# Performance work log

Hardware: AMD Instinct MI355X
Metric: run time of the kernel (lower is better)

Reference implementation:

```python
import jax, jax.numpy as jnp
import numpy as np

B, N, D, H, L, FF, CLS = 32, 196, 768, 12, 12, 3072, 1000
HD = D // H
EPS = 1e-5


def setup_inputs() -> dict:
    key = jax.random.key(0)
    ks = jax.random.split(key, 8)
    s = 0.02
    return dict(
        x=jax.random.normal(ks[0], (B, N, D), jnp.float32),
        pos_emb=jax.random.normal(ks[1], (1, N, D), jnp.float32) * 0.2,
        qkv_w=jax.random.normal(ks[2], (L, D, 3 * D), jnp.float32) * s,
        qkv_b=jnp.zeros((L, 3 * D), jnp.float32),
        proj_w=jax.random.normal(ks[3], (L, D, D), jnp.float32) * s,
        proj_b=jnp.zeros((L, D), jnp.float32),
        lin1_w=jax.random.normal(ks[4], (L, D, FF), jnp.float32) * s,
        lin1_b=jnp.zeros((L, FF), jnp.float32),
        lin2_w=jax.random.normal(ks[5], (L, FF, D), jnp.float32) * s,
        lin2_b=jnp.zeros((L, D), jnp.float32),
        pre_ln_w=jnp.ones((L, D), jnp.float32),
        pre_ln_b=jnp.zeros((L, D), jnp.float32),
        norm1_w=jnp.ones((L, D), jnp.float32),
        norm1_b=jnp.zeros((L, D), jnp.float32),
        attn_ln_w=jnp.ones((L, H, N, N), jnp.float32),
        attn_ln_b=jnp.zeros((L, H, N, N), jnp.float32),
        final_ln_w=jnp.ones((D,), jnp.float32),
        final_ln_b=jnp.zeros((D,), jnp.float32),
        pool_w=jax.random.normal(ks[6], (D, 1), jnp.float32) * s,
        pool_b=jnp.zeros((1,), jnp.float32),
        fc_w=jax.random.normal(ks[7], (D, CLS), jnp.float32) * s,
        fc_b=jnp.zeros((CLS,), jnp.float32),
    )


def _ln(x, w, b):
    mu = x.mean(-1, keepdims=True)
    var = ((x - mu) ** 2).mean(-1, keepdims=True)
    return (x - mu) * jax.lax.rsqrt(var + EPS) * w + b


def _forward(x, pos_emb, qkv_w, qkv_b, proj_w, proj_b, lin1_w, lin1_b,
             lin2_w, lin2_b, pre_ln_w, pre_ln_b, norm1_w, norm1_b,
             attn_ln_w, attn_ln_b, final_ln_w, final_ln_b,
             pool_w, pool_b, fc_w, fc_b):
    h = x + pos_emb  # (B,N,D)
    params = dict(qw=qkv_w, qb=qkv_b, pw=proj_w, pb=proj_b,
                  l1w=lin1_w, l1b=lin1_b, l2w=lin2_w, l2b=lin2_b,
                  prew=pre_ln_w, preb=pre_ln_b, n1w=norm1_w, n1b=norm1_b,
                  aw=attn_ln_w, ab=attn_ln_b)

    def step(carry, p):
        src, _ = carry
        y = _ln(src, p['prew'], p['preb'])
        qkv = (y @ p['qw'] + p['qb']).reshape(B, N, 3, H, HD)
        qkv = qkv.transpose(2, 0, 3, 1, 4)  # (3,B,H,N,HD)
        q, k, v = qkv[0], qkv[1], qkv[2]
        # grassmanian_point: project each head vector onto the unit sphere
        q = q / jnp.linalg.norm(q, axis=-1, keepdims=True)
        k = k / jnp.linalg.norm(k, axis=-1, keepdims=True)
        # ||q_i outer k_j||^2 over head_dim == sum_d q_id^2 * k_jd^2
        attn = jnp.einsum('bhid,bhjd->bhij', q * q, k * k)  # (B,H,N,N)
        # LayerNorm over (H,N,N) per batch element
        mu = attn.mean(axis=(1, 2, 3), keepdims=True)
        var = ((attn - mu) ** 2).mean(axis=(1, 2, 3), keepdims=True)
        attn = (attn - mu) * jax.lax.rsqrt(var + EPS) * p['aw'] + p['ab']
        out = jnp.einsum('bhij,bhjd->bhid', attn, v)
        out = out.transpose(0, 2, 1, 3).reshape(B, N, D)
        out = out @ p['pw'] + p['pb']
        src = _ln(src + out, p['n1w'], p['n1b'])
        ff = jax.nn.gelu(src @ p['l1w'] + p['l1b'], approximate=False)
        ff = ff @ p['l2w'] + p['l2b']
        return (src + ff, attn), None

    init = (h, jnp.zeros((B, H, N, N), x.dtype))
    (src, attn), _ = jax.lax.scan(step, init, params)
    xf = _ln(src, final_ln_w, final_ln_b)
    a = jax.nn.softmax(xf @ pool_w + pool_b, axis=1)  # (B,N,1) sequence pooling
    pooled = jnp.einsum('bnk,bnd->bd', a, xf)
    logits = pooled @ fc_w + fc_b
    return logits, attn


def reference(x, pos_emb, qkv_w, qkv_b, proj_w, proj_b, lin1_w, lin1_b,
              lin2_w, lin2_b, pre_ln_w, pre_ln_b, norm1_w, norm1_b,
              attn_ln_w, attn_ln_b, final_ln_w, final_ln_b,
              pool_w, pool_b, fc_w, fc_b):
    return _forward(x, pos_emb, qkv_w, qkv_b, proj_w, proj_b, lin1_w, lin1_b,
                    lin2_w, lin2_b, pre_ln_w, pre_ln_b, norm1_w, norm1_b,
                    attn_ln_w, attn_ln_b, final_ln_w, final_ln_b,
                    pool_w, pool_b, fc_w, fc_b)
```

## Files before the change

### kernel.cpp

```cpp
#include <hip/hip_runtime.h>
#include <hip/hip_bf16.h>

typedef unsigned short u16;
typedef __bf16 bf16x8 __attribute__((ext_vector_type(8)));
typedef _Float16 f16x8 __attribute__((ext_vector_type(8)));
typedef float f32x4 __attribute__((ext_vector_type(4)));
typedef u16 u16x8 __attribute__((ext_vector_type(8)));
typedef u16 u16x4 __attribute__((ext_vector_type(4)));

#define B_ 32
#define N_ 196
#define D_ 768
#define H_ 12
#define L_ 12
#define FF_ 3072
#define CLS_ 1000
#define HD_ 64
#define BH_ 384
#define NTOK_ 6272
#define NP_ 224
#define ATTN_PER_B_ 460992
#define NN_ 38416

__device__ inline u16 f2bf(float f){
    __bf16 h = (__bf16)f;
    return __builtin_bit_cast(u16, h);
}
__device__ inline float bf2f(u16 u){
    __bf16 h = __builtin_bit_cast(__bf16, u);
    return (float)h;
}
__device__ inline void split3(float v, u16& s0, u16& s1, u16& s2){
    s0 = f2bf(v);
    float r = v - bf2f(s0);
    s1 = f2bf(r);
    r = r - bf2f(s1);
    s2 = f2bf(r);
}
__device__ inline u16 f2h(float f){
    _Float16 h = (_Float16)f;
    return __builtin_bit_cast(u16, h);
}
__device__ inline float h2f(u16 u){
    _Float16 h = __builtin_bit_cast(_Float16, u);
    return (float)h;
}
__device__ inline void split2h(float v, u16& h0, u16& h1){
    h0 = f2h(v);
    h1 = f2h(v - h2f(h0));
}


__global__ __launch_bounds__(256)
void addpos_kernel(const float* __restrict__ x, const float* __restrict__ pos,
                   float* __restrict__ src){
    size_t gid = (size_t)blockIdx.x * 256 + threadIdx.x;
    size_t e = gid * 4;
    size_t tok = e / D_;
    size_t d = e % D_;
    size_t pe = (tok % N_) * D_ + d;
    float4 a = *(const float4*)(x + e);
    float4 p = *(const float4*)(pos + pe);
    float4 o = make_float4(a.x + p.x, a.y + p.y, a.z + p.z, a.w + p.w);
    *(float4*)(src + e) = o;
}

__global__ __launch_bounds__(256)
void wtrans_kernel(const float* __restrict__ in, u16* __restrict__ o0,
                   u16* __restrict__ o1, int K, int Nn){
    __shared__ float t[32][33];
    int n0 = blockIdx.x * 32, k0 = blockIdx.y * 32;
    int tx = threadIdx.x & 31, ty = threadIdx.x >> 5;
#pragma unroll
    for (int r = 0; r < 4; ++r)
        t[ty + 8*r][tx] = in[(size_t)(k0 + ty + 8*r) * Nn + n0 + tx];
    __syncthreads();
#pragma unroll
    for (int r = 0; r < 4; ++r){
        float v = t[tx][ty + 8*r];
        size_t oi = (size_t)(n0 + ty + 8*r) * K + k0 + tx;
        u16 a, b;
        split2h(v, a, b);
        o0[oi] = a; o1[oi] = b;
    }
}


__global__ __launch_bounds__(256)
void ln_row(const float* __restrict__ in, const float* __restrict__ w,
            const float* __restrict__ bb, float* __restrict__ outF,
            u16* __restrict__ o0, u16* __restrict__ o1){
    int row = blockIdx.x, tid = threadIdx.x;
    const float* base = in + (size_t)row * D_;
    float x0 = base[tid], x1 = base[tid + 256], x2 = base[tid + 512];
    float s = x0 + x1 + x2;
    float q = x0*x0 + x1*x1 + x2*x2;
    __shared__ float red[8];
    for (int o = 32; o > 0; o >>= 1){ s += __shfl_down(s, o); q += __shfl_down(q, o); }
    if ((tid & 63) == 0){ red[tid >> 6] = s; red[4 + (tid >> 6)] = q; }
    __syncthreads();
    s = red[0] + red[1] + red[2] + red[3];
    q = red[4] + red[5] + red[6] + red[7];
    float mu = s * (1.f / D_);
    float rv = rsqrtf(q * (1.f / D_) - mu * mu + 1e-5f);
#pragma unroll
    for (int t = 0; t < 3; ++t){
        int c = tid + t * 256;
        float x = (t == 0 ? x0 : (t == 1 ? x1 : x2));
        float val = (x - mu) * rv * w[c] + bb[c];
        size_t oi = (size_t)row * D_ + c;
        if (outF) outF[oi] = val;
        if (o0){
            u16 a, b;
            split2h(val, a, b);
            o0[oi] = a; o1[oi] = b;
        }
    }
}


template<int EPI>
__global__ __launch_bounds__(256)
void gemm_f16s2(const u16* __restrict__ A0, const u16* __restrict__ A1,
                const u16* __restrict__ B0, const u16* __restrict__ B1,
                const float* __restrict__ bias, const float* __restrict__ res,
                float* __restrict__ outF, u16* __restrict__ oH,
                u16* __restrict__ oL, int M, int Nn, int K){
    __shared__ u16 Lds[2][4][128 * 32];
    const int tid = threadIdx.x;
    const int w = tid >> 6, l = tid & 63;
    const int wr = w >> 1, wc = w & 1;
    const int nwg = gridDim.x;
    const int nbx = Nn >> 7;
    const int orig = blockIdx.x;
    const int qq = nwg >> 3, rr = nwg & 7;
    const int xcd = orig & 7, local = orig >> 3;
    const int wg = (xcd < rr ? xcd * (qq + 1) : rr * (qq + 1) + (xcd - rr) * qq) + local;
    const int m0 = (wg / nbx) * 128, n0 = (wg % nbx) * 128;
    const u16* gsrc = (w == 0 ? A0 : w == 1 ? A1 : w == 2 ? B0 : B1);
    const int rowbase = (w < 2 ? m0 : n0);
    const int lq = (l & 3) ^ ((l >> 3) & 3);
    const u16* gp = gsrc + (size_t)(rowbase + (l >> 2)) * K + lq * 8;
    const size_t gstep = (size_t)16 * K;
    f32x4 acc[4][4] = {};
    const int arow = l & 15;
    const int qsel = l >> 4;
    const int nsteps = K >> 5;

    auto stage = [&](int buf, int k0){
        u16* lbuf = &Lds[buf][w][0];
        const u16* gpk = gp + k0;
#pragma unroll
        for (int i = 0; i < 8; ++i){
            __builtin_amdgcn_global_load_lds(
                (const __attribute__((address_space(1))) unsigned int*)gpk,
                (__attribute__((address_space(3))) unsigned int*)(lbuf + i * 512),
                16, 0, 0);
            gpk += gstep;
        }
    };

    stage(0, 0);
    for (int step = 0; step < nsteps; ++step){
        const int cur = step & 1;
        __syncthreads();
        if (step + 1 < nsteps) stage(1 - cur, (step + 1) << 5);
        f16x8 a0[4], a1[4], b0[4], b1[4];
#pragma unroll
        for (int m = 0; m < 4; ++m){
            int row = wr * 64 + m * 16 + arow;
            int off = row * 32 + ((qsel ^ ((row >> 1) & 3)) * 8);
            a0[m] = __builtin_bit_cast(f16x8, *(const u16x8*)&Lds[cur][0][off]);
            a1[m] = __builtin_bit_cast(f16x8, *(const u16x8*)&Lds[cur][1][off]);
        }
#pragma unroll
        for (int n = 0; n < 4; ++n){
            int row = wc * 64 + n * 16 + arow;
            int off = row * 32 + ((qsel ^ ((row >> 1) & 3)) * 8);
            b0[n] = __builtin_bit_cast(f16x8, *(const u16x8*)&Lds[cur][2][off]);
            b1[n] = __builtin_bit_cast(f16x8, *(const u16x8*)&Lds[cur][3][off]);
        }
#pragma unroll
        for (int m = 0; m < 4; ++m)
#pragma unroll
            for (int n = 0; n < 4; ++n){
                acc[m][n] = __builtin_amdgcn_mfma_f32_16x16x32_f16(a1[m], b0[n], acc[m][n], 0, 0, 0);
                acc[m][n] = __builtin_amdgcn_mfma_f32_16x16x32_f16(a0[m], b1[n], acc[m][n], 0, 0, 0);
                acc[m][n] = __builtin_amdgcn_mfma_f32_16x16x32_f16(a0[m], b0[n], acc[m][n], 0, 0, 0);
            }
    }
    const int r4 = (l >> 4) * 4, c16 = l & 15;
#pragma unroll
    for (int m = 0; m < 4; ++m){
#pragma unroll
        for (int n = 0; n < 4; ++n){
            int colg = n0 + wc*64 + n*16 + c16;
            float bv = bias[colg];
#pragma unroll
            for (int r = 0; r < 4; ++r){
                int rowg = m0 + wr*64 + m*16 + r4 + r;
                size_t oi = (size_t)rowg * Nn + colg;
                float v = acc[m][n][r] + bv;
                if (EPI == 0){
                    outF[oi] = v;
                } else if (EPI == 1){
                    v = 0.5f * v * (1.0f + erff(v * 0.70710678118654752f));
                    u16 a, b;
                    split2h(v, a, b);
                    oH[oi] = a; oL[oi] = b;
                } else {
                    outF[oi] = v + res[oi];
                }
            }
        }
    }
}


__global__ __launch_bounds__(256)
void qkprep_kernel(const float* __restrict__ QKV,
                   u16* __restrict__ Q0, u16* __restrict__ Q1, u16* __restrict__ Q2,
                   u16* __restrict__ K0, u16* __restrict__ K1, u16* __restrict__ K2,
                   u16* __restrict__ VT0, u16* __restrict__ VT1, u16* __restrict__ VT2){
    __shared__ float vbuf[NP_][65];
    int bh = blockIdx.x;
    int b = bh / H_, h = bh % H_;
    int w = threadIdx.x >> 6, l = threadIdx.x & 63;
    size_t base = (size_t)bh * (NP_ * HD_);
    for (int n = w; n < NP_; n += 4){
        size_t oi = base + (size_t)n * HD_ + l;
        if (n < N_){
            const float* row = QKV + (size_t)(b * N_ + n) * (3 * D_) + h * HD_;
            float qv = row[l], kv = row[D_ + l], vv = row[2 * D_ + l];
            double qs = (double)qv * (double)qv, ks = (double)kv * (double)kv;
            double qr = qs, kr = ks;
            for (int o = 32; o > 0; o >>= 1){ qr += __shfl_xor(qr, o); kr += __shfl_xor(kr, o); }
            float q2 = (float)(qs / qr), k2 = (float)(ks / kr);
            u16 a, bb, c;
            split3(q2, a, bb, c);
            Q0[oi] = a; Q1[oi] = bb; Q2[oi] = c;
            split3(k2, a, bb, c);
            K0[oi] = a; K1[oi] = bb; K2[oi] = c;
            vbuf[n][l] = vv;
        } else {
            Q0[oi] = 0; Q1[oi] = 0; Q2[oi] = 0;
            K0[oi] = 0; K1[oi] = 0; K2[oi] = 0;
            vbuf[n][l] = 0.f;
        }
    }
    __syncthreads();
    size_t vtb = (size_t)bh * (HD_ * NP_);
    for (int idx = threadIdx.x; idx < HD_ * NP_; idx += 256){
        int d = idx / NP_, n = idx % NP_;
        u16 a, bb, c;
        split3(vbuf[n][d], a, bb, c);
        VT0[vtb + idx] = a; VT1[vtb + idx] = bb; VT2[vtb + idx] = c;
    }
}


#define SPAD 72

__global__ __launch_bounds__(256)
void score_mfma3(const u16* __restrict__ Q0, const u16* __restrict__ Q1,
                 const u16* __restrict__ Q2,
                 const u16* __restrict__ K0, const u16* __restrict__ K1,
                 const u16* __restrict__ K2,
                 float* __restrict__ S){
    __shared__ u16 Ql[3][32][SPAD];
    __shared__ u16 Kl[3][32][SPAD];
    int i0 = blockIdx.x * 32;
    int bh = blockIdx.y;
    int tid = threadIdx.x;
    size_t base = (size_t)bh * (NP_ * HD_);
    {
        int r = tid >> 3, q = tid & 7;
        size_t src = base + (size_t)(i0 + r) * HD_ + q * 8;
        *(u16x8*)&Ql[0][r][q * 8] = *(const u16x8*)(Q0 + src);
        *(u16x8*)&Ql[1][r][q * 8] = *(const u16x8*)(Q1 + src);
        *(u16x8*)&Ql[2][r][q * 8] = *(const u16x8*)(Q2 + src);
    }
    const int w = tid >> 6, l = tid & 63;
    const int wm = w >> 1, wn = w & 1;
    const int arow = l & 15, kg0 = (l >> 4) * 8;
    const int r4 = (l >> 4) * 4, c16 = l & 15;
    for (int jt = 0; jt < 7; ++jt){
        __syncthreads();
        {
            int r = tid >> 3, q = tid & 7;
            size_t src = base + (size_t)(jt * 32 + r) * HD_ + q * 8;
            *(u16x8*)&Kl[0][r][q * 8] = *(const u16x8*)(K0 + src);
            *(u16x8*)&Kl[1][r][q * 8] = *(const u16x8*)(K1 + src);
            *(u16x8*)&Kl[2][r][q * 8] = *(const u16x8*)(K2 + src);
        }
        __syncthreads();
        f32x4 acc = {};
#pragma unroll
        for (int kk = 0; kk < 2; ++kk){
            int kg = kk * 32 + kg0;
            bf16x8 a0 = __builtin_bit_cast(bf16x8, *(const u16x8*)&Ql[0][wm*16 + arow][kg]);
            bf16x8 a1 = __builtin_bit_cast(bf16x8, *(const u16x8*)&Ql[1][wm*16 + arow][kg]);
            bf16x8 a2 = __builtin_bit_cast(bf16x8, *(const u16x8*)&Ql[2][wm*16 + arow][kg]);
            bf16x8 b0 = __builtin_bit_cast(bf16x8, *(const u16x8*)&Kl[0][wn*16 + arow][kg]);
            bf16x8 b1 = __builtin_bit_cast(bf16x8, *(const u16x8*)&Kl[1][wn*16 + arow][kg]);
            bf16x8 b2 = __builtin_bit_cast(bf16x8, *(const u16x8*)&Kl[2][wn*16 + arow][kg]);
            acc = __builtin_amdgcn_mfma_f32_16x16x32_bf16(a2, b0, acc, 0, 0, 0);
            acc = __builtin_amdgcn_mfma_f32_16x16x32_bf16(a1, b1, acc, 0, 0, 0);
            acc = __builtin_amdgcn_mfma_f32_16x16x32_bf16(a0, b2, acc, 0, 0, 0);
            acc = __builtin_amdgcn_mfma_f32_16x16x32_bf16(a1, b0, acc, 0, 0, 0);
            acc = __builtin_amdgcn_mfma_f32_16x16x32_bf16(a0, b1, acc, 0, 0, 0);
            acc = __builtin_amdgcn_mfma_f32_16x16x32_bf16(a0, b0, acc, 0, 0, 0);
        }
#pragma unroll
        for (int r = 0; r < 4; ++r){
            int i = i0 + wm * 16 + r4 + r;
            int j = jt * 32 + wn * 16 + c16;
            if (i < N_ && j < N_)
                S[((size_t)bh * N_ + i) * N_ + j] = acc[r];
        }
    }
}


__global__ __launch_bounds__(256)
void statsA_kernel(const float* __restrict__ S, double* __restrict__ part1){
    int b = blockIdx.y, c = blockIdx.x;
    const float* base = S + (size_t)b * ATTN_PER_B_ + (size_t)c * 7203;
    double s = 0.0;
    for (int i = threadIdx.x; i < 7203; i += 256)
        s += (double)base[i];
    __shared__ double red[4];
    for (int o = 32; o > 0; o >>= 1) s += __shfl_down(s, o);
    if ((threadIdx.x & 63) == 0) red[threadIdx.x >> 6] = s;
    __syncthreads();
    if (threadIdx.x == 0) part1[b * 64 + c] = red[0] + red[1] + red[2] + red[3];
}

__global__ __launch_bounds__(64)
void reduceMu_kernel(const double* __restrict__ part1, double* __restrict__ MU){
    int b = blockIdx.x;
    double s = part1[b * 64 + threadIdx.x];
    for (int o = 32; o > 0; o >>= 1) s += __shfl_down(s, o);
    if (threadIdx.x == 0) MU[b] = s / (double)ATTN_PER_B_;
}

__global__ __launch_bounds__(256)
void statsB_kernel(const float* __restrict__ S, const double* __restrict__ MU,
                   double* __restrict__ part2){
    int b = blockIdx.y, c = blockIdx.x;
    double mu = MU[b];
    const float* base = S + (size_t)b * ATTN_PER_B_ + (size_t)c * 7203;
    double q = 0.0;
    for (int i = threadIdx.x; i < 7203; i += 256){
        double d = (double)base[i] - mu;
        q += d * d;
    }
    __shared__ double red[4];
    for (int o = 32; o > 0; o >>= 1) q += __shfl_down(q, o);
    if ((threadIdx.x & 63) == 0) red[threadIdx.x >> 6] = q;
    __syncthreads();
    if (threadIdx.x == 0) part2[b * 64 + c] = red[0] + red[1] + red[2] + red[3];
}

__global__ __launch_bounds__(64)
void reduceR_kernel(const double* __restrict__ part2, const double* __restrict__ MU,
                    float2* __restrict__ musig){
    int b = blockIdx.x;
    double q = part2[b * 64 + threadIdx.x];
    for (int o = 32; o > 0; o >>= 1) q += __shfl_down(q, o);
    if (threadIdx.x == 0){
        double var = q / (double)ATTN_PER_B_;
        musig[b] = make_float2((float)MU[b], (float)(1.0 / sqrt(var + 1e-5)));
    }
}


__global__ __launch_bounds__(256)
void attnnorm_pad(float* __restrict__ S, const float* __restrict__ wv,
                  const float* __restrict__ bv, const float2* __restrict__ musig,
                  u16* __restrict__ AS0, u16* __restrict__ AS1, u16* __restrict__ AS2){
    int gid = blockIdx.x * 256 + threadIdx.x;
    int jg = gid % 56;
    int rem = gid / 56;
    int i = rem % NP_;
    int bh = rem / NP_;
    int b = bh / H_, h = bh % H_;
    float2 ms = musig[b];
    u16x4 p0, p1, p2;
#pragma unroll
    for (int t = 0; t < 4; ++t){
        int j = jg * 4 + t;
        float val = 0.f;
        if (i < N_ && j < N_){
            size_t si = ((size_t)bh * N_ + i) * N_ + j;
            size_t wi = ((size_t)h * N_ + i) * N_ + j;
            float s = S[si];
            val = (s - ms.x) * ms.y * wv[wi] + bv[wi];
            S[si] = val;
        }
        u16 a, bb, c;
        split3(val, a, bb, c);
        p0[t] = a; p1[t] = bb; p2[t] = c;
    }
    size_t oo = (size_t)bh * (NP_ * NP_) + (size_t)i * NP_ + jg * 4;
    *(u16x4*)&AS0[oo] = p0;
    *(u16x4*)&AS1[oo] = p1;
    *(u16x4*)&AS2[oo] = p2;
}


__global__ __launch_bounds__(256)
void pv_mfma3(const u16* __restrict__ AS0, const u16* __restrict__ AS1,
              const u16* __restrict__ AS2,
              const u16* __restrict__ VT0, const u16* __restrict__ VT1,
              const u16* __restrict__ VT2,
              u16* __restrict__ PA0, u16* __restrict__ PA1){
    __shared__ u16 Al[3][32][40];
    __shared__ u16 Vl[3][64][40];
    int i0 = blockIdx.x * 32;
    int bh = blockIdx.y;
    int b = bh / H_, h = bh % H_;
    int tid = threadIdx.x;
    size_t abase = (size_t)bh * (NP_ * NP_) + (size_t)i0 * NP_;
    size_t vbase = (size_t)bh * (HD_ * NP_);
    const int w = tid >> 6, l = tid & 63;
    const int arow = l & 15, kg0 = (l >> 4) * 8;
    const int r4 = (l >> 4) * 4, c16 = l & 15;
    f32x4 acc[2] = {};
    for (int k0 = 0; k0 < NP_; k0 += 32){
        __syncthreads();
        for (int c = tid; c < 384; c += 256){
            int s = c >> 7, rem = c & 127;
            int r = rem >> 2, q = rem & 3;
            const u16* src = (s == 0 ? AS0 : (s == 1 ? AS1 : AS2));
            *(u16x8*)&Al[s][r][q * 8] = *(const u16x8*)(src + abase + (size_t)r * NP_ + k0 + q * 8);
        }
        for (int c = tid; c < 768; c += 256){
            int s = c >> 8, rem = c & 255;
            int r = rem >> 2, q = rem & 3;
            const u16* src = (s == 0 ? VT0 : (s == 1 ? VT1 : VT2));
            *(u16x8*)&Vl[s][r][q * 8] = *(const u16x8*)(src + vbase + (size_t)r * NP_ + k0 + q * 8);
        }
        __syncthreads();
        bf16x8 a0[2], a1[2], a2[2];
#pragma unroll
        for (int m = 0; m < 2; ++m){
            a0[m] = __builtin_bit_cast(bf16x8, *(const u16x8*)&Al[0][m*16 + arow][kg0]);
            a1[m] = __builtin_bit_cast(bf16x8, *(const u16x8*)&Al[1][m*16 + arow][kg0]);
            a2[m] = __builtin_bit_cast(bf16x8, *(const u16x8*)&Al[2][m*16 + arow][kg0]);
        }
        bf16x8 b0 = __builtin_bit_cast(bf16x8, *(const u16x8*)&Vl[0][w*16 + arow][kg0]);
        bf16x8 b1 = __builtin_bit_cast(bf16x8, *(const u16x8*)&Vl[1][w*16 + arow][kg0]);
        bf16x8 b2 = __builtin_bit_cast(bf16x8, *(const u16x8*)&Vl[2][w*16 + arow][kg0]);
#pragma unroll
        for (int m = 0; m < 2; ++m){
            acc[m] = __builtin_amdgcn_mfma_f32_16x16x32_bf16(a2[m], b0, acc[m], 0, 0, 0);
            acc[m] = __builtin_amdgcn_mfma_f32_16x16x32_bf16(a1[m], b1, acc[m], 0, 0, 0);
            acc[m] = __builtin_amdgcn_mfma_f32_16x16x32_bf16(a0[m], b2, acc[m], 0, 0, 0);
            acc[m] = __builtin_amdgcn_mfma_f32_16x16x32_bf16(a1[m], b0, acc[m], 0, 0, 0);
            acc[m] = __builtin_amdgcn_mfma_f32_16x16x32_bf16(a0[m], b1, acc[m], 0, 0, 0);
            acc[m] = __builtin_amdgcn_mfma_f32_16x16x32_bf16(a0[m], b0, acc[m], 0, 0, 0);
        }
    }
#pragma unroll
    for (int m = 0; m < 2; ++m)
#pragma unroll
        for (int r = 0; r < 4; ++r){
            int i = i0 + m * 16 + r4 + r;
            if (i < N_){
                size_t oi = ((size_t)b * N_ + i) * D_ + h * HD_ + w * 16 + c16;
                u16 s0, s1;
                split2h(acc[m][r], s0, s1);
                PA0[oi] = s0; PA1[oi] = s1;
            }
        }
}


__global__ __launch_bounds__(256)
void rowdot_kernel(const float* __restrict__ xf, const float* __restrict__ pw,
                   const float* __restrict__ pb, float* __restrict__ sraw){
    int row = blockIdx.x, tid = threadIdx.x;
    const float* base = xf + (size_t)row * D_;
    float s = base[tid] * pw[tid] + base[tid + 256] * pw[tid + 256] + base[tid + 512] * pw[tid + 512];
    __shared__ float red[4];
    for (int o = 32; o > 0; o >>= 1) s += __shfl_xor(s, o);
    if ((tid & 63) == 0) red[tid >> 6] = s;
    __syncthreads();
    if (tid == 0) sraw[row] = red[0] + red[1] + red[2] + red[3] + pb[0];
}

__global__ __launch_bounds__(256)
void softmax196_kernel(const float* __restrict__ sraw, float* __restrict__ aw){
    int b = blockIdx.x, tid = threadIdx.x;
    __shared__ float red[8];
    float v = (tid < N_) ? sraw[b * N_ + tid] : -3.0e38f;
    float m = v;
    for (int o = 32; o > 0; o >>= 1) m = fmaxf(m, __shfl_xor(m, o));
    if ((tid & 63) == 0) red[tid >> 6] = m;
    __syncthreads();
    float M = fmaxf(fmaxf(red[0], red[1]), fmaxf(red[2], red[3]));
    float e = (tid < N_) ? expf(v - M) : 0.f;
    float s = e;
    for (int o = 32; o > 0; o >>= 1) s += __shfl_xor(s, o);
    if ((tid & 63) == 0) red[4 + (tid >> 6)] = s;
    __syncthreads();
    float S = red[4] + red[5] + red[6] + red[7];
    if (tid < N_) aw[b * N_ + tid] = e / S;
}

__global__ __launch_bounds__(256)
void poolmat_kernel(const float* __restrict__ aw, const float* __restrict__ xf,
                    float* __restrict__ pooled){
    int b = blockIdx.y;
    int d = blockIdx.x * 256 + threadIdx.x;
    float acc = 0.f;
    for (int n = 0; n < N_; ++n)
        acc += aw[b * N_ + n] * xf[((size_t)b * N_ + n) * D_ + d];
    pooled[b * D_ + d] = acc;
}

__global__ __launch_bounds__(256)
void fc_kernel(const float* __restrict__ pooled, const float* __restrict__ fw,
               const float* __restrict__ fb, float* __restrict__ out){
    int b = blockIdx.y;
    int c = blockIdx.x * 256 + threadIdx.x;
    if (c >= CLS_) return;
    float acc = fb[c];
    for (int d = 0; d < D_; ++d)
        acc += pooled[b * D_ + d] * fw[(size_t)d * CLS_ + c];
    out[b * CLS_ + c] = acc;
}

__global__ __launch_bounds__(256)
void zero_logits(float* __restrict__ out){
    out[blockIdx.x * 256 + threadIdx.x] = 0.f;
}


extern "C" void kernel_launch(void* const* d_in, const int* in_sizes, int n_in,
                              void* d_out, int out_size, void* d_ws, size_t ws_size,
                              hipStream_t stream){
    const float* x        = (const float*)d_in[0];
    const float* pos_emb  = (const float*)d_in[1];
    const float* qkv_w    = (const float*)d_in[2];
    const float* qkv_b    = (const float*)d_in[3];
    const float* proj_w   = (const float*)d_in[4];
    const float* proj_b   = (const float*)d_in[5];
    const float* lin1_w   = (const float*)d_in[6];
    const float* lin1_b   = (const float*)d_in[7];
    const float* lin2_w   = (const float*)d_in[8];
    const float* lin2_b   = (const float*)d_in[9];
    const float* pre_ln_w = (const float*)d_in[10];
    const float* pre_ln_b = (const float*)d_in[11];
    const float* norm1_w  = (const float*)d_in[12];
    const float* norm1_b  = (const float*)d_in[13];
    const float* attn_ln_w= (const float*)d_in[14];
    const float* attn_ln_b= (const float*)d_in[15];
    const float* fln_w    = (const float*)d_in[16];
    const float* fln_b    = (const float*)d_in[17];
    const float* pool_w   = (const float*)d_in[18];
    const float* pool_b   = (const float*)d_in[19];
    const float* fc_w     = (const float*)d_in[20];
    const float* fc_b     = (const float*)d_in[21];

    float* dout = (float*)d_out;
    float* S = dout + (size_t)B_ * CLS_;

    char* ws = (char*)d_ws;
    size_t off = 0;
    auto alloc = [&](size_t bytes)->char*{
        char* p = ws + off;
        off += (bytes + 255) & ~(size_t)255;
        return p;
    };
    float* SRC   = (float*)alloc((size_t)NTOK_ * D_ * 4);
    float* Yb    = (float*)alloc((size_t)NTOK_ * D_ * 4);
    float* TMP   = (float*)alloc((size_t)NTOK_ * D_ * 4);
    float* QKV   = (float*)alloc((size_t)NTOK_ * 3 * D_ * 4);
    u16*   A0    = (u16*)  alloc((size_t)NTOK_ * D_ * 2);
    u16*   A1    = (u16*)  alloc((size_t)NTOK_ * D_ * 2);
    u16*   W0    = (u16*)  alloc((size_t)FF_ * D_ * 2);
    u16*   W1    = (u16*)  alloc((size_t)FF_ * D_ * 2);
    u16*   F0    = (u16*)  alloc((size_t)NTOK_ * FF_ * 2);
    u16*   F1    = (u16*)  alloc((size_t)NTOK_ * FF_ * 2);
    u16*   F2    = (u16*)  alloc((size_t)NTOK_ * FF_ * 2);
    u16*   Q0b   = (u16*)  alloc((size_t)BH_ * NP_ * HD_ * 2);
    u16*   Q1b   = (u16*)  alloc((size_t)BH_ * NP_ * HD_ * 2);
    u16*   Q2b   = (u16*)  alloc((size_t)BH_ * NP_ * HD_ * 2);
    u16*   K0b   = (u16*)  alloc((size_t)BH_ * NP_ * HD_ * 2);
    u16*   K1b   = (u16*)  alloc((size_t)BH_ * NP_ * HD_ * 2);
    u16*   K2b   = (u16*)  alloc((size_t)BH_ * NP_ * HD_ * 2);
    u16*   VT0   = (u16*)  alloc((size_t)BH_ * HD_ * NP_ * 2);
    u16*   VT1   = (u16*)  alloc((size_t)BH_ * HD_ * NP_ * 2);
    u16*   VT2   = (u16*)  alloc((size_t)BH_ * HD_ * NP_ * 2);
    double* P1   = (double*)alloc((size_t)B_ * 64 * 8);
    double* P2   = (double*)alloc((size_t)B_ * 64 * 8);
    double* MU   = (double*)alloc((size_t)B_ * 8);
    float2* MUSIG= (float2*)alloc((size_t)B_ * 8);
    float* SRAW  = (float*)alloc((size_t)NTOK_ * 4);
    float* AW    = (float*)alloc((size_t)NTOK_ * 4);
    float* POOLED= (float*)alloc((size_t)B_ * D_ * 4);
    u16* AS0 = F0, *AS1 = F1, *AS2 = F2;

    if (ws_size < off){
        zero_logits<<<(B_ * CLS_) / 256, 256, 0, stream>>>(dout);
        return;
    }

    const int cvt_blocks = NTOK_ * D_ / (256 * 4);
    const int an_blocks = (int)((size_t)BH_ * NP_ * NP_ / (256 * 4));

    addpos_kernel<<<cvt_blocks, 256, 0, stream>>>(x, pos_emb, SRC);

    for (int l = 0; l < L_; ++l){
        const float* qw  = qkv_w  + (size_t)l * D_ * 3 * D_;
        const float* qb  = qkv_b  + (size_t)l * 3 * D_;
        const float* pw  = proj_w + (size_t)l * D_ * D_;
        const float* pb  = proj_b + (size_t)l * D_;
        const float* l1w = lin1_w + (size_t)l * D_ * FF_;
        const float* l1b = lin1_b + (size_t)l * FF_;
        const float* l2w = lin2_w + (size_t)l * FF_ * D_;
        const float* l2b = lin2_b + (size_t)l * D_;
        const float* prw = pre_ln_w + (size_t)l * D_;
        const float* prb = pre_ln_b + (size_t)l * D_;
        const float* n1w = norm1_w + (size_t)l * D_;
        const float* n1b = norm1_b + (size_t)l * D_;
        const float* awl = attn_ln_w + (size_t)l * H_ * N_ * N_;
        const float* abl = attn_ln_b + (size_t)l * H_ * N_ * N_;

        ln_row<<<NTOK_, 256, 0, stream>>>(SRC, prw, prb, nullptr, A0, A1);
        wtrans_kernel<<<dim3(3 * D_ / 32, D_ / 32), 256, 0, stream>>>(qw, W0, W1, D_, 3 * D_);
        gemm_f16s2<0><<<(3 * D_ / 128) * (NTOK_ / 128), 256, 0, stream>>>(
            A0, A1, W0, W1, qb, nullptr, QKV, nullptr, nullptr, NTOK_, 3 * D_, D_);
        qkprep_kernel<<<BH_, 256, 0, stream>>>(QKV, Q0b, Q1b, Q2b, K0b, K1b, K2b,
                                               VT0, VT1, VT2);
        score_mfma3<<<dim3(7, BH_), 256, 0, stream>>>(Q0b, Q1b, Q2b, K0b, K1b, K2b, S);
        statsA_kernel<<<dim3(64, B_), 256, 0, stream>>>(S, P1);
        reduceMu_kernel<<<B_, 64, 0, stream>>>(P1, MU);
        statsB_kernel<<<dim3(64, B_), 256, 0, stream>>>(S, MU, P2);
        reduceR_kernel<<<B_, 64, 0, stream>>>(P2, MU, MUSIG);
        attnnorm_pad<<<an_blocks, 256, 0, stream>>>(S, awl, abl, MUSIG, AS0, AS1, AS2);
        pv_mfma3<<<dim3(7, BH_), 256, 0, stream>>>(AS0, AS1, AS2, VT0, VT1, VT2, A0, A1);
        wtrans_kernel<<<dim3(D_ / 32, D_ / 32), 256, 0, stream>>>(pw, W0, W1, D_, D_);
        gemm_f16s2<2><<<(D_ / 128) * (NTOK_ / 128), 256, 0, stream>>>(
            A0, A1, W0, W1, pb, SRC, TMP, nullptr, nullptr, NTOK_, D_, D_);
        ln_row<<<NTOK_, 256, 0, stream>>>(TMP, n1w, n1b, SRC, A0, A1);
        wtrans_kernel<<<dim3(FF_ / 32, D_ / 32), 256, 0, stream>>>(l1w, W0, W1, D_, FF_);
        gemm_f16s2<1><<<(FF_ / 128) * (NTOK_ / 128), 256, 0, stream>>>(
            A0, A1, W0, W1, l1b, nullptr, nullptr, F0, F1, NTOK_, FF_, D_);
        wtrans_kernel<<<dim3(D_ / 32, FF_ / 32), 256, 0, stream>>>(l2w, W0, W1, FF_, D_);
        gemm_f16s2<2><<<(D_ / 128) * (NTOK_ / 128), 256, 0, stream>>>(
            F0, F1, W0, W1, l2b, SRC, SRC, nullptr, nullptr, NTOK_, D_, FF_);
    }

    ln_row<<<NTOK_, 256, 0, stream>>>(SRC, fln_w, fln_b, Yb, nullptr, nullptr);
    rowdot_kernel<<<NTOK_, 256, 0, stream>>>(Yb, pool_w, pool_b, SRAW);
    softmax196_kernel<<<B_, 256, 0, stream>>>(SRAW, AW);
    poolmat_kernel<<<dim3(D_ / 256, B_), 256, 0, stream>>>(AW, Yb, POOLED);
    fc_kernel<<<dim3((CLS_ + 255) / 256, B_), 256, 0, stream>>>(POOLED, fc_w, fc_b, dout);
}
```

Baseline: 8.326 ms.

## Fuse attention stats into score kernel, use 2-term fp16 split for PV

```diff
diff --git a/kernel.cpp b/kernel.cpp
--- a/kernel.cpp
+++ b/kernel.cpp
@@ -221,7 +221,7 @@
 void qkprep_kernel(const float* __restrict__ QKV,
                    u16* __restrict__ Q0, u16* __restrict__ Q1, u16* __restrict__ Q2,
                    u16* __restrict__ K0, u16* __restrict__ K1, u16* __restrict__ K2,
-                   u16* __restrict__ VT0, u16* __restrict__ VT1, u16* __restrict__ VT2){
+                   u16* __restrict__ VT0, u16* __restrict__ VT1){
     __shared__ float vbuf[NP_][65];
     int bh = blockIdx.x;
     int b = bh / H_, h = bh % H_;
@@ -252,9 +252,9 @@
     size_t vtb = (size_t)bh * (HD_ * NP_);
     for (int idx = threadIdx.x; idx < HD_ * NP_; idx += 256){
         int d = idx / NP_, n = idx % NP_;
-        u16 a, bb, c;
-        split3(vbuf[n][d], a, bb, c);
-        VT0[vtb + idx] = a; VT1[vtb + idx] = bb; VT2[vtb + idx] = c;
+        u16 a, bb;
+        split2h(vbuf[n][d], a, bb);
+        VT0[vtb + idx] = a; VT1[vtb + idx] = bb;
     }
 }
 
@@ -266,9 +266,10 @@
                  const u16* __restrict__ Q2,
                  const u16* __restrict__ K0, const u16* __restrict__ K1,
                  const u16* __restrict__ K2,
-                 float* __restrict__ S){
+                 float* __restrict__ S, double2* __restrict__ part){
     __shared__ u16 Ql[3][32][SPAD];
     __shared__ u16 Kl[3][32][SPAD];
+    __shared__ double red2[8];
     int i0 = blockIdx.x * 32;
     int bh = blockIdx.y;
     int tid = threadIdx.x;
@@ -284,6 +285,7 @@
     const int wm = w >> 1, wn = w & 1;
     const int arow = l & 15, kg0 = (l >> 4) * 8;
     const int r4 = (l >> 4) * 4, c16 = l & 15;
+    double dsum = 0.0, dsq = 0.0;
     for (int jt = 0; jt < 7; ++jt){
         __syncthreads();
         {
@@ -315,70 +317,50 @@
         for (int r = 0; r < 4; ++r){
             int i = i0 + wm * 16 + r4 + r;
             int j = jt * 32 + wn * 16 + c16;
-            if (i < N_ && j < N_)
-                S[((size_t)bh * N_ + i) * N_ + j] = acc[r];
-        }
-    }
-}
-
-
-__global__ __launch_bounds__(256)
-void statsA_kernel(const float* __restrict__ S, double* __restrict__ part1){
-    int b = blockIdx.y, c = blockIdx.x;
-    const float* base = S + (size_t)b * ATTN_PER_B_ + (size_t)c * 7203;
-    double s = 0.0;
-    for (int i = threadIdx.x; i < 7203; i += 256)
-        s += (double)base[i];
-    __shared__ double red[4];
-    for (int o = 32; o > 0; o >>= 1) s += __shfl_down(s, o);
-    if ((threadIdx.x & 63) == 0) red[threadIdx.x >> 6] = s;
-    __syncthreads();
-    if (threadIdx.x == 0) part1[b * 64 + c] = red[0] + red[1] + red[2] + red[3];
+            if (i < N_ && j < N_){
+                float v = acc[r];
+                S[((size_t)bh * N_ + i) * N_ + j] = v;
+                dsum += (double)v;
+                dsq += (double)v * (double)v;
+            }
+        }
+    }
+    for (int o = 32; o > 0; o >>= 1){
+        dsum += __shfl_down(dsum, o);
+        dsq  += __shfl_down(dsq, o);
+    }
+    __syncthreads();
+    if ((tid & 63) == 0){ red2[tid >> 6] = dsum; red2[4 + (tid >> 6)] = dsq; }
+    __syncthreads();
+    if (tid == 0){
+        int b = bh / H_, h = bh % H_;
+        part[(size_t)b * 84 + h * 7 + blockIdx.x] =
+            make_double2(red2[0] + red2[1] + red2[2] + red2[3],
+                         red2[4] + red2[5] + red2[6] + red2[7]);
+    }
 }
 
 __global__ __launch_bounds__(64)
-void reduceMu_kernel(const double* __restrict__ part1, double* __restrict__ MU){
-    int b = blockIdx.x;
-    double s = part1[b * 64 + threadIdx.x];
-    for (int o = 32; o > 0; o >>= 1) s += __shfl_down(s, o);
-    if (threadIdx.x == 0) MU[b] = s / (double)ATTN_PER_B_;
-}
-
-__global__ __launch_bounds__(256)
-void statsB_kernel(const float* __restrict__ S, const double* __restrict__ MU,
-                   double* __restrict__ part2){
-    int b = blockIdx.y, c = blockIdx.x;
-    double mu = MU[b];
-    const float* base = S + (size_t)b * ATTN_PER_B_ + (size_t)c * 7203;
-    double q = 0.0;
-    for (int i = threadIdx.x; i < 7203; i += 256){
-        double d = (double)base[i] - mu;
-        q += d * d;
-    }
-    __shared__ double red[4];
-    for (int o = 32; o > 0; o >>= 1) q += __shfl_down(q, o);
-    if ((threadIdx.x & 63) == 0) red[threadIdx.x >> 6] = q;
-    __syncthreads();
-    if (threadIdx.x == 0) part2[b * 64 + c] = red[0] + red[1] + red[2] + red[3];
-}
-
-__global__ __launch_bounds__(64)
-void reduceR_kernel(const double* __restrict__ part2, const double* __restrict__ MU,
-                    float2* __restrict__ musig){
-    int b = blockIdx.x;
-    double q = part2[b * 64 + threadIdx.x];
-    for (int o = 32; o > 0; o >>= 1) q += __shfl_down(q, o);
-    if (threadIdx.x == 0){
-        double var = q / (double)ATTN_PER_B_;
-        musig[b] = make_float2((float)MU[b], (float)(1.0 / sqrt(var + 1e-5)));
-    }
-}
-
-
-__global__ __launch_bounds__(256)
-void attnnorm_pad(float* __restrict__ S, const float* __restrict__ wv,
+void reduceMS_kernel(const double2* __restrict__ part, float2* __restrict__ musig){
+    int b = blockIdx.x, tid = threadIdx.x;
+    double s = 0.0, q = 0.0;
+    for (int i = tid; i < 84; i += 64){
+        double2 p = part[(size_t)b * 84 + i];
+        s += p.x; q += p.y;
+    }
+    for (int o = 32; o > 0; o >>= 1){ s += __shfl_down(s, o); q += __shfl_down(q, o); }
+    if (tid == 0){
+        double mu = s / (double)ATTN_PER_B_;
+        double var = q / (double)ATTN_PER_B_ - mu * mu;
+        musig[b] = make_float2((float)mu, (float)(1.0 / sqrt(var + 1e-5)));
+    }
+}
+
+
+__global__ __launch_bounds__(256)
+void attnnorm_f16(float* __restrict__ S, const float* __restrict__ wv,
                   const float* __restrict__ bv, const float2* __restrict__ musig,
-                  u16* __restrict__ AS0, u16* __restrict__ AS1, u16* __restrict__ AS2){
+                  u16* __restrict__ AS0, u16* __restrict__ AS1, int writeS){
     int gid = blockIdx.x * 256 + threadIdx.x;
     int jg = gid % 56;
     int rem = gid / 56;
@@ -386,7 +368,7 @@
     int bh = rem / NP_;
     int b = bh / H_, h = bh % H_;
     float2 ms = musig[b];
-    u16x4 p0, p1, p2;
+    u16x4 p0, p1;
 #pragma unroll
     for (int t = 0; t < 4; ++t){
         int j = jg * 4 + t;
@@ -396,27 +378,24 @@
             size_t wi = ((size_t)h * N_ + i) * N_ + j;
             float s = S[si];
             val = (s - ms.x) * ms.y * wv[wi] + bv[wi];
-            S[si] = val;
-        }
-        u16 a, bb, c;
-        split3(val, a, bb, c);
-        p0[t] = a; p1[t] = bb; p2[t] = c;
+            if (writeS) S[si] = val;
+        }
+        u16 a, bb;
+        split2h(val, a, bb);
+        p0[t] = a; p1[t] = bb;
     }
     size_t oo = (size_t)bh * (NP_ * NP_) + (size_t)i * NP_ + jg * 4;
     *(u16x4*)&AS0[oo] = p0;
     *(u16x4*)&AS1[oo] = p1;
-    *(u16x4*)&AS2[oo] = p2;
-}
-
-
-__global__ __launch_bounds__(256)
-void pv_mfma3(const u16* __restrict__ AS0, const u16* __restrict__ AS1,
-              const u16* __restrict__ AS2,
+}
+
+
+__global__ __launch_bounds__(256)
+void pv_f16s2(const u16* __restrict__ AS0, const u16* __restrict__ AS1,
               const u16* __restrict__ VT0, const u16* __restrict__ VT1,
-              const u16* __restrict__ VT2,
               u16* __restrict__ PA0, u16* __restrict__ PA1){
-    __shared__ u16 Al[3][32][40];
-    __shared__ u16 Vl[3][64][40];
+    __shared__ u16 Al[2][32][40];
+    __shared__ u16 Vl[2][64][40];
     int i0 = blockIdx.x * 32;
     int bh = blockIdx.y;
     int b = bh / H_, h = bh % H_;
@@ -429,37 +408,35 @@
     f32x4 acc[2] = {};
     for (int k0 = 0; k0 < NP_; k0 += 32){
         __syncthreads();
-        for (int c = tid; c < 384; c += 256){
-            int s = c >> 7, rem = c & 127;
+        {
+            int s = tid >> 7, rem = tid & 127;
             int r = rem >> 2, q = rem & 3;
-            const u16* src = (s == 0 ? AS0 : (s == 1 ? AS1 : AS2));
+            const u16* src = (s == 0 ? AS0 : AS1);
             *(u16x8*)&Al[s][r][q * 8] = *(const u16x8*)(src + abase + (size_t)r * NP_ + k0 + q * 8);
         }
-        for (int c = tid; c < 768; c += 256){
+#pragma unroll
+        for (int it = 0; it < 2; ++it){
+            int c = tid + it * 256;
             int s = c >> 8, rem = c & 255;
             int r = rem >> 2, q = rem & 3;
-            const u16* src = (s == 0 ? VT0 : (s == 1 ? VT1 : VT2));
+            const u16* src = (s == 0 ? VT0 : VT1);
             *(u16x8*)&Vl[s][r][q * 8] = *(const u16x8*)(src + vbase + (size_t)r * NP_ + k0 + q * 8);
         }
         __syncthreads();
-        bf16x8 a0[2], a1[2], a2[2];
+        f16x8 a0[2], a1[2];
 #pragma unroll
         for (int m = 0; m < 2; ++m){
-            a0[m] = __builtin_bit_cast(bf16x8, *(const u16x8*)&Al[0][m*16 + arow][kg0]);
-            a1[m] = __builtin_bit_cast(bf16x8, *(const u16x8*)&Al[1][m*16 + arow][kg0]);
-            a2[m] = __builtin_bit_cast(bf16x8, *(const u16x8*)&Al[2][m*16 + arow][kg0]);
-        }
-        bf16x8 b0 = __builtin_bit_cast(bf16x8, *(const u16x8*)&Vl[0][w*16 + arow][kg0]);
-        bf16x8 b1 = __builtin_bit_cast(bf16x8, *(const u16x8*)&Vl[1][w*16 + arow][kg0]);
-        bf16x8 b2 = __builtin_bit_cast(bf16x8, *(const u16x8*)&Vl[2][w*16 + arow][kg0]);
+            a0[m] = __builtin_bit_cast(f16x8, *(const u16x8*)&Al[0][m*16 + arow][kg0]);
+            a1[m] = __builtin_bit_cast(f16x8, *(const u16x8*)&Al[1][m*16 + arow][kg0]);
+        }
+        f16x8 b0 = __builtin_bit_cast(f16x8, *(const u16x8*)&Vl[0][w*16 + arow][kg0]);
+        f16x8 b1 = __builtin_bit_cast(f16x8, *(const u16x8*)&Vl[1][w*16 + arow][kg0]);
 #pragma unroll
         for (int m = 0; m < 2; ++m){
-            acc[m] = __builtin_amdgcn_mfma_f32_16x16x32_bf16(a2[m], b0, acc[m], 0, 0, 0);
-            acc[m] = __builtin_amdgcn_mfma_f32_16x16x32_bf16(a1[m], b1, acc[m], 0, 0, 0);
-            acc[m] = __builtin_amdgcn_mfma_f32_16x16x32_bf16(a0[m], b2, acc[m], 0, 0, 0);
-            acc[m] = __builtin_amdgcn_mfma_f32_16x16x32_bf16(a1[m], b0, acc[m], 0, 0, 0);
-            acc[m] = __builtin_amdgcn_mfma_f32_16x16x32_bf16(a0[m], b1, acc[m], 0, 0, 0);
-            acc[m] = __builtin_amdgcn_mfma_f32_16x16x32_bf16(a0[m], b0, acc[m], 0, 0, 0);
+            acc[m] = __builtin_amdgcn_mfma_f32_16x16x32_f16(a1[m], b1, acc[m], 0, 0, 0);
+            acc[m] = __builtin_amdgcn_mfma_f32_16x16x32_f16(a1[m], b0, acc[m], 0, 0, 0);
+            acc[m] = __builtin_amdgcn_mfma_f32_16x16x32_f16(a0[m], b1, acc[m], 0, 0, 0);
+            acc[m] = __builtin_amdgcn_mfma_f32_16x16x32_f16(a0[m], b0, acc[m], 0, 0, 0);
         }
     }
 #pragma unroll
@@ -584,7 +561,6 @@
     u16*   W1    = (u16*)  alloc((size_t)FF_ * D_ * 2);
     u16*   F0    = (u16*)  alloc((size_t)NTOK_ * FF_ * 2);
     u16*   F1    = (u16*)  alloc((size_t)NTOK_ * FF_ * 2);
-    u16*   F2    = (u16*)  alloc((size_t)NTOK_ * FF_ * 2);
     u16*   Q0b   = (u16*)  alloc((size_t)BH_ * NP_ * HD_ * 2);
     u16*   Q1b   = (u16*)  alloc((size_t)BH_ * NP_ * HD_ * 2);
     u16*   Q2b   = (u16*)  alloc((size_t)BH_ * NP_ * HD_ * 2);
@@ -593,15 +569,12 @@
     u16*   K2b   = (u16*)  alloc((size_t)BH_ * NP_ * HD_ * 2);
     u16*   VT0   = (u16*)  alloc((size_t)BH_ * HD_ * NP_ * 2);
     u16*   VT1   = (u16*)  alloc((size_t)BH_ * HD_ * NP_ * 2);
-    u16*   VT2   = (u16*)  alloc((size_t)BH_ * HD_ * NP_ * 2);
-    double* P1   = (double*)alloc((size_t)B_ * 64 * 8);
-    double* P2   = (double*)alloc((size_t)B_ * 64 * 8);
-    double* MU   = (double*)alloc((size_t)B_ * 8);
+    double2* PART= (double2*)alloc((size_t)B_ * 84 * 16);
     float2* MUSIG= (float2*)alloc((size_t)B_ * 8);
     float* SRAW  = (float*)alloc((size_t)NTOK_ * 4);
     float* AW    = (float*)alloc((size_t)NTOK_ * 4);
     float* POOLED= (float*)alloc((size_t)B_ * D_ * 4);
-    u16* AS0 = F0, *AS1 = F1, *AS2 = F2;
+    u16* AS0 = F0, *AS1 = F1;
 
     if (ws_size < off){
         zero_logits<<<(B_ * CLS_) / 256, 256, 0, stream>>>(dout);
@@ -634,14 +607,13 @@
         gemm_f16s2<0><<<(3 * D_ / 128) * (NTOK_ / 128), 256, 0, stream>>>(
             A0, A1, W0, W1, qb, nullptr, QKV, nullptr, nullptr, NTOK_, 3 * D_, D_);
         qkprep_kernel<<<BH_, 256, 0, stream>>>(QKV, Q0b, Q1b, Q2b, K0b, K1b, K2b,
-                                               VT0, VT1, VT2);
-        score_mfma3<<<dim3(7, BH_), 256, 0, stream>>>(Q0b, Q1b, Q2b, K0b, K1b, K2b, S);
-        statsA_kernel<<<dim3(64, B_), 256, 0, stream>>>(S, P1);
-        reduceMu_kernel<<<B_, 64, 0, stream>>>(P1, MU);
-        statsB_kernel<<<dim3(64, B_), 256, 0, stream>>>(S, MU, P2);
-        reduceR_kernel<<<B_, 64, 0, stream>>>(P2, MU, MUSIG);
-        attnnorm_pad<<<an_blocks, 256, 0, stream>>>(S, awl, abl, MUSIG, AS0, AS1, AS2);
-        pv_mfma3<<<dim3(7, BH_), 256, 0, stream>>>(AS0, AS1, AS2, VT0, VT1, VT2, A0, A1);
+                                               VT0, VT1);
+        score_mfma3<<<dim3(7, BH_), 256, 0, stream>>>(Q0b, Q1b, Q2b, K0b, K1b, K2b,
+                                                      S, PART);
+        reduceMS_kernel<<<B_, 64, 0, stream>>>(PART, MUSIG);
+        attnnorm_f16<<<an_blocks, 256, 0, stream>>>(S, awl, abl, MUSIG, AS0, AS1,
+                                                    l == L_ - 1 ? 1 : 0);
+        pv_f16s2<<<dim3(7, BH_), 256, 0, stream>>>(AS0, AS1, VT0, VT1, A0, A1);
         wtrans_kernel<<<dim3(D_ / 32, D_ / 32), 256, 0, stream>>>(pw, W0, W1, D_, D_);
         gemm_f16s2<2><<<(D_ / 128) * (NTOK_ / 128), 256, 0, stream>>>(
             A0, A1, W0, W1, pb, SRC, TMP, nullptr, nullptr, NTOK_, D_, D_);
```

After: 7.306 ms. 12.2% less time.
